# Kernel optimization log

Hardware: AMD Instinct MI355X
Metric: run time of the kernel (lower is better)

Reference implementation:

```python
import jax, jax.numpy as jnp
import numpy as np

NUM_LOCAL = 4      # num_local_experts
E_TOTAL = 8        # local + unpopular experts
HIDDEN = 1024
FFN = 4 * HIDDEN
CAP = 2048         # tokens (capacity) per expert
D0 = 1             # leading dim of inputs / output_tensor


def setup_inputs() -> dict:
    key = jax.random.key(0)
    k_in, k_w0, k_w3 = jax.random.split(key, 3)
    inputs = jax.random.normal(k_in, (D0, E_TOTAL, CAP, HIDDEN), dtype=jnp.float32)
    # gating-activity indicator per expert; all-ones -> all unpopular experts active
    output_tensor = jnp.ones((D0, E_TOTAL), dtype=jnp.float32)
    # stacked per-expert MLP weights (torch Linear convention: [out, in])
    w0 = jax.random.normal(k_w0, (E_TOTAL, FFN, HIDDEN), dtype=jnp.float32) * 0.02
    w3 = jax.random.normal(k_w3, (E_TOTAL, HIDDEN, FFN), dtype=jnp.float32) * 0.02
    return {"output_tensor": output_tensor, "inputs": inputs, "w0": w0, "w3": w3}


def reference(output_tensor, inputs, w0, w3):
    # Grouped 2-layer MLP per expert: x @ w0^T -> GELU -> @ w3^T
    # b: D0, e: expert, c: capacity, d: hidden, f: ffn
    h = jnp.einsum('becd,efd->becf', inputs, w0)
    h = jax.nn.gelu(h, approximate=False)  # torch nn.GELU default = exact erf
    out = jnp.einsum('becf,edf->becd', h, w3)
    # unpopular experts with zero activity produce zeros (scatter-into-zeros combine)
    unpop_mask = jnp.sum(output_tensor[:, NUM_LOCAL:], axis=0) != 0  # [E_unpop]
    full_mask = jnp.concatenate(
        [jnp.ones((NUM_LOCAL,), dtype=bool), unpop_mask])  # locals always computed
    out = out * full_mask[None, :, None, None].astype(out.dtype)
    return out
```

## Files before the change

### kernel.cpp

```cpp
#include <hip/hip_runtime.h>
#include <math.h>

#define E_TOTAL 8
#define NUM_LOCAL 4
#define HIDDEN 1024
#define FFN 4096
#define CAP 2048

typedef unsigned short ushort_t;
typedef __attribute__((ext_vector_type(8))) short short8;
typedef __attribute__((ext_vector_type(8))) unsigned short u16x8;
typedef __attribute__((ext_vector_type(4))) float f32x4;

__device__ __forceinline__ unsigned short f2bf(float f) {
  unsigned int u = __float_as_uint(f);
  u += 0x7FFFu + ((u >> 16) & 1u);
  return (unsigned short)(u >> 16);
}

__device__ __forceinline__ void gload_lds16(const void* g, void* l) {
  __builtin_amdgcn_global_load_lds(
      (const __attribute__((address_space(1))) void*)g,
      (__attribute__((address_space(3))) void*)l,
      16, 0, 0);
}

__global__ __launch_bounds__(256) void cvt_kernel(const float4* __restrict__ s,
                                                  u16x8* __restrict__ d) {
  const size_t i = (size_t)blockIdx.x * 256 + threadIdx.x;
  float4 a = s[2 * i], b = s[2 * i + 1];
  u16x8 o;
  o[0] = f2bf(a.x); o[1] = f2bf(a.y); o[2] = f2bf(a.z); o[3] = f2bf(a.w);
  o[4] = f2bf(b.x); o[5] = f2bf(b.y); o[6] = f2bf(b.z); o[7] = f2bf(b.w);
  d[i] = o;
}

template <int M, int N, int K, bool GELU_OUT>
__global__ __launch_bounds__(256, 2) void gemm_nt(
    const ushort_t* __restrict__ A, const ushort_t* __restrict__ B,
    void* __restrict__ Cout, const float* __restrict__ ot, int d0) {
  __shared__ ushort_t lds_a[128 * 64];
  __shared__ ushort_t lds_b[128 * 64];

  const int e = blockIdx.z;
  const int bm = blockIdx.x * 128;
  const int bn = blockIdx.y * 128;
  const int t = threadIdx.x;
  const int wave = t >> 6, lane = t & 63;
  const int wr = wave >> 1, wc = wave & 1;
  const int quad = lane >> 4, l16 = lane & 15;
  const int r8 = lane >> 3;
  const int s8 = lane & 7;
  const int g8 = (s8 + r8) & 7;

  const ushort_t* Ag = A + (size_t)e * M * K + (size_t)(bm + r8) * K + g8 * 8;
  const ushort_t* Bg = B + (size_t)e * N * K + (size_t)(bn + r8) * K + g8 * 8;

  f32x4 acc[4][4];
#pragma unroll
  for (int i = 0; i < 4; ++i)
#pragma unroll
    for (int j = 0; j < 4; ++j) {
      f32x4 z = {0.f, 0.f, 0.f, 0.f};
      acc[i][j] = z;
    }

  for (int kb = 0; kb < K / 64; ++kb) {
    const size_t ko = (size_t)kb * 64;
#pragma unroll
    for (int j = 0; j < 4; ++j) {
      const int R = (j * 4 + wave) * 8;
      gload_lds16(Ag + ko + (size_t)R * K, &lds_a[R * 64]);
      gload_lds16(Bg + ko + (size_t)R * K, &lds_b[R * 64]);
    }
    __syncthreads();

#pragma unroll
    for (int ks = 0; ks < 2; ++ks) {
      short8 af[4], bfr[4];
      const int c = ks * 4 + quad;
#pragma unroll
      for (int i = 0; i < 4; ++i) {
        const int ra = wr * 64 + i * 16 + l16;
        const int rb = wc * 64 + i * 16 + l16;
        af[i]  = *(const short8*)&lds_a[ra * 64 + ((c - ra) & 7) * 8];
        bfr[i] = *(const short8*)&lds_b[rb * 64 + ((c - rb) & 7) * 8];
      }
#pragma unroll
      for (int mi = 0; mi < 4; ++mi)
#pragma unroll
        for (int ni = 0; ni < 4; ++ni)
          acc[mi][ni] = __builtin_amdgcn_mfma_f32_16x16x32_bf16(
              af[mi], bfr[ni], acc[mi][ni], 0, 0, 0);
    }
    __syncthreads();
  }

  if (GELU_OUT) {
    ushort_t* C = (ushort_t*)Cout + (size_t)e * M * N +
                  (size_t)(bm + wr * 64) * N + (bn + wc * 64);
#pragma unroll
    for (int mi = 0; mi < 4; ++mi)
#pragma unroll
      for (int r = 0; r < 4; ++r) {
        const int row = mi * 16 + quad * 4 + r;
#pragma unroll
        for (int ni = 0; ni < 4; ++ni) {
          float v = acc[mi][ni][r];
          v = 0.5f * v * (1.f + erff(v * 0.70710678118654752f));
          C[(size_t)row * N + ni * 16 + l16] = f2bf(v);
        }
      }
  } else {
    float mask = 1.f;
    if (e >= NUM_LOCAL) {
      float s = 0.f;
      for (int b = 0; b < d0; ++b) s += ot[b * E_TOTAL + e];
      mask = (s != 0.f) ? 1.f : 0.f;
    }
    float* C = (float*)Cout + (size_t)e * M * N +
               (size_t)(bm + wr * 64) * N + (bn + wc * 64);
#pragma unroll
    for (int mi = 0; mi < 4; ++mi)
#pragma unroll
      for (int r = 0; r < 4; ++r) {
        const int row = mi * 16 + quad * 4 + r;
#pragma unroll
        for (int ni = 0; ni < 4; ++ni)
          C[(size_t)row * N + ni * 16 + l16] = acc[mi][ni][r] * mask;
      }
  }
}

extern "C" void kernel_launch(void* const* d_in, const int* in_sizes, int n_in,
                              void* d_out, int out_size, void* d_ws,
                              size_t ws_size, hipStream_t stream) {
  const float* ot = (const float*)d_in[0];
  const float* x  = (const float*)d_in[1];
  const float* w0 = (const float*)d_in[2];
  const float* w3 = (const float*)d_in[3];
  const int d0 = in_sizes[0] / E_TOTAL;

  char* ws = (char*)d_ws;
  ushort_t* xb  = (ushort_t*)ws;
  ushort_t* w0b = (ushort_t*)(ws + (size_t)32 * 1024 * 1024);
  ushort_t* w3b = (ushort_t*)ws;
  ushort_t* h   = (ushort_t*)(ws + (size_t)96 * 1024 * 1024);

  const int nx = E_TOTAL * CAP * HIDDEN;
  const int nw = E_TOTAL * FFN * HIDDEN;

  cvt_kernel<<<nx / (256 * 8), 256, 0, stream>>>((const float4*)x, (u16x8*)xb);
  cvt_kernel<<<nw / (256 * 8), 256, 0, stream>>>((const float4*)w0, (u16x8*)w0b);

  gemm_nt<CAP, FFN, HIDDEN, true>
      <<<dim3(CAP / 128, FFN / 128, E_TOTAL), 256, 0, stream>>>(
          xb, w0b, h, nullptr, d0);

  cvt_kernel<<<nw / (256 * 8), 256, 0, stream>>>((const float4*)w3, (u16x8*)w3b);

  gemm_nt<CAP, HIDDEN, FFN, false>
      <<<dim3(CAP / 128, HIDDEN / 128, E_TOTAL), 256, 0, stream>>>(
          h, w3b, d_out, ot, d0);
}
```

Measured before the change: 677.0 us.

## Switch GEMMs to 32x32x16 MFMA and merge bf16 conversions into one kernel

The GEMM inner loop now issues 32x32x16 bf16 MFMA instructions on 2x2 accumulator tiles instead of 16x16x32 on 4x4 tiles. That halves the LDS fragment loads per MFMA and uses the larger matrix-core op, with the epilogue index mapping rewritten to match. When the workspace is large enough, the three fp32-to-bf16 conversions run as one kernel with separate buffers, which removes two launches. The 32-wide output stores have a different coalescing pattern, and the larger workspace path depends on ws_size.

```diff
diff --git a/kernel.cpp b/kernel.cpp
--- a/kernel.cpp
+++ b/kernel.cpp
@@ -10,7 +10,7 @@
 typedef unsigned short ushort_t;
 typedef __attribute__((ext_vector_type(8))) short short8;
 typedef __attribute__((ext_vector_type(8))) unsigned short u16x8;
-typedef __attribute__((ext_vector_type(4))) float f32x4;
+typedef __attribute__((ext_vector_type(16))) float f32x16;
 
 __device__ __forceinline__ unsigned short f2bf(float f) {
   unsigned int u = __float_as_uint(f);
@@ -23,6 +23,26 @@
       (const __attribute__((address_space(1))) void*)g,
       (__attribute__((address_space(3))) void*)l,
       16, 0, 0);
+}
+
+__global__ __launch_bounds__(256) void cvt3_kernel(
+    const float4* __restrict__ x, const float4* __restrict__ w0,
+    const float4* __restrict__ w3, u16x8* __restrict__ xb,
+    u16x8* __restrict__ w0b, u16x8* __restrict__ w3b) {
+  const int NX8 = E_TOTAL * CAP * HIDDEN / 8;
+  const int NW8 = E_TOTAL * FFN * HIDDEN / 8;
+  const int i = blockIdx.x * 256 + threadIdx.x;
+  const float4* s;
+  u16x8* d;
+  int j;
+  if (i < NX8) { s = x; d = xb; j = i; }
+  else if (i < NX8 + NW8) { s = w0; d = w0b; j = i - NX8; }
+  else { s = w3; d = w3b; j = i - NX8 - NW8; }
+  float4 a = s[2 * (size_t)j], b = s[2 * (size_t)j + 1];
+  u16x8 o;
+  o[0] = f2bf(a.x); o[1] = f2bf(a.y); o[2] = f2bf(a.z); o[3] = f2bf(a.w);
+  o[4] = f2bf(b.x); o[5] = f2bf(b.y); o[6] = f2bf(b.z); o[7] = f2bf(b.w);
+  d[j] = o;
 }
 
 __global__ __launch_bounds__(256) void cvt_kernel(const float4* __restrict__ s,
@@ -48,7 +68,7 @@
   const int t = threadIdx.x;
   const int wave = t >> 6, lane = t & 63;
   const int wr = wave >> 1, wc = wave & 1;
-  const int quad = lane >> 4, l16 = lane & 15;
+  const int l32 = lane & 31, h5 = lane >> 5;
   const int r8 = lane >> 3;
   const int s8 = lane & 7;
   const int g8 = (s8 + r8) & 7;
@@ -56,14 +76,13 @@
   const ushort_t* Ag = A + (size_t)e * M * K + (size_t)(bm + r8) * K + g8 * 8;
   const ushort_t* Bg = B + (size_t)e * N * K + (size_t)(bn + r8) * K + g8 * 8;
 
-  f32x4 acc[4][4];
-#pragma unroll
-  for (int i = 0; i < 4; ++i)
-#pragma unroll
-    for (int j = 0; j < 4; ++j) {
-      f32x4 z = {0.f, 0.f, 0.f, 0.f};
-      acc[i][j] = z;
-    }
+  f32x16 acc[2][2];
+#pragma unroll
+  for (int i = 0; i < 2; ++i)
+#pragma unroll
+    for (int j = 0; j < 2; ++j)
+#pragma unroll
+      for (int r = 0; r < 16; ++r) acc[i][j][r] = 0.f;
 
   for (int kb = 0; kb < K / 64; ++kb) {
     const size_t ko = (size_t)kb * 64;
@@ -76,39 +95,40 @@
     __syncthreads();
 
 #pragma unroll
-    for (int ks = 0; ks < 2; ++ks) {
-      short8 af[4], bfr[4];
-      const int c = ks * 4 + quad;
-#pragma unroll
-      for (int i = 0; i < 4; ++i) {
-        const int ra = wr * 64 + i * 16 + l16;
-        const int rb = wc * 64 + i * 16 + l16;
-        af[i]  = *(const short8*)&lds_a[ra * 64 + ((c - ra) & 7) * 8];
-        bfr[i] = *(const short8*)&lds_b[rb * 64 + ((c - rb) & 7) * 8];
+    for (int ks = 0; ks < 4; ++ks) {
+      const int c = ks * 2 + h5;
+      short8 af[2], bfr[2];
+#pragma unroll
+      for (int mi = 0; mi < 2; ++mi) {
+        const int ra = wr * 64 + mi * 32 + l32;
+        const int rb = wc * 64 + mi * 32 + l32;
+        af[mi]  = *(const short8*)&lds_a[ra * 64 + ((c - ra) & 7) * 8];
+        bfr[mi] = *(const short8*)&lds_b[rb * 64 + ((c - rb) & 7) * 8];
       }
 #pragma unroll
-      for (int mi = 0; mi < 4; ++mi)
-#pragma unroll
-        for (int ni = 0; ni < 4; ++ni)
-          acc[mi][ni] = __builtin_amdgcn_mfma_f32_16x16x32_bf16(
+      for (int mi = 0; mi < 2; ++mi)
+#pragma unroll
+        for (int ni = 0; ni < 2; ++ni)
+          acc[mi][ni] = __builtin_amdgcn_mfma_f32_32x32x16_bf16(
               af[mi], bfr[ni], acc[mi][ni], 0, 0, 0);
     }
     __syncthreads();
   }
 
   if (GELU_OUT) {
-    ushort_t* C = (ushort_t*)Cout + (size_t)e * M * N +
-                  (size_t)(bm + wr * 64) * N + (bn + wc * 64);
-#pragma unroll
-    for (int mi = 0; mi < 4; ++mi)
-#pragma unroll
-      for (int r = 0; r < 4; ++r) {
-        const int row = mi * 16 + quad * 4 + r;
-#pragma unroll
-        for (int ni = 0; ni < 4; ++ni) {
+    ushort_t* C = (ushort_t*)Cout + (size_t)e * M * N;
+#pragma unroll
+    for (int mi = 0; mi < 2; ++mi)
+#pragma unroll
+      for (int ni = 0; ni < 2; ++ni) {
+        const int rbase = bm + wr * 64 + mi * 32;
+        const int cbase = bn + wc * 64 + ni * 32;
+#pragma unroll
+        for (int r = 0; r < 16; ++r) {
+          const int row = rbase + (r & 3) + 8 * (r >> 2) + 4 * h5;
           float v = acc[mi][ni][r];
           v = 0.5f * v * (1.f + erff(v * 0.70710678118654752f));
-          C[(size_t)row * N + ni * 16 + l16] = f2bf(v);
+          C[(size_t)row * N + cbase + l32] = f2bf(v);
         }
       }
   } else {
@@ -118,16 +138,18 @@
       for (int b = 0; b < d0; ++b) s += ot[b * E_TOTAL + e];
       mask = (s != 0.f) ? 1.f : 0.f;
     }
-    float* C = (float*)Cout + (size_t)e * M * N +
-               (size_t)(bm + wr * 64) * N + (bn + wc * 64);
-#pragma unroll
-    for (int mi = 0; mi < 4; ++mi)
-#pragma unroll
-      for (int r = 0; r < 4; ++r) {
-        const int row = mi * 16 + quad * 4 + r;
-#pragma unroll
-        for (int ni = 0; ni < 4; ++ni)
-          C[(size_t)row * N + ni * 16 + l16] = acc[mi][ni][r] * mask;
+    float* C = (float*)Cout + (size_t)e * M * N;
+#pragma unroll
+    for (int mi = 0; mi < 2; ++mi)
+#pragma unroll
+      for (int ni = 0; ni < 2; ++ni) {
+        const int rbase = bm + wr * 64 + mi * 32;
+        const int cbase = bn + wc * 64 + ni * 32;
+#pragma unroll
+        for (int r = 0; r < 16; ++r) {
+          const int row = rbase + (r & 3) + 8 * (r >> 2) + 4 * h5;
+          C[(size_t)row * N + cbase + l32] = acc[mi][ni][r] * mask;
+        }
       }
   }
 }
@@ -142,24 +164,43 @@
   const int d0 = in_sizes[0] / E_TOTAL;
 
   char* ws = (char*)d_ws;
-  ushort_t* xb  = (ushort_t*)ws;
-  ushort_t* w0b = (ushort_t*)(ws + (size_t)32 * 1024 * 1024);
-  ushort_t* w3b = (ushort_t*)ws;
-  ushort_t* h   = (ushort_t*)(ws + (size_t)96 * 1024 * 1024);
-
+  const size_t MB = 1024 * 1024;
   const int nx = E_TOTAL * CAP * HIDDEN;
   const int nw = E_TOTAL * FFN * HIDDEN;
 
-  cvt_kernel<<<nx / (256 * 8), 256, 0, stream>>>((const float4*)x, (u16x8*)xb);
-  cvt_kernel<<<nw / (256 * 8), 256, 0, stream>>>((const float4*)w0, (u16x8*)w0b);
-
-  gemm_nt<CAP, FFN, HIDDEN, true>
-      <<<dim3(CAP / 128, FFN / 128, E_TOTAL), 256, 0, stream>>>(
-          xb, w0b, h, nullptr, d0);
-
-  cvt_kernel<<<nw / (256 * 8), 256, 0, stream>>>((const float4*)w3, (u16x8*)w3b);
-
-  gemm_nt<CAP, HIDDEN, FFN, false>
-      <<<dim3(CAP / 128, HIDDEN / 128, E_TOTAL), 256, 0, stream>>>(
-          h, w3b, d_out, ot, d0);
-}
+  if (ws_size >= 288 * MB) {
+    ushort_t* xb  = (ushort_t*)ws;
+    ushort_t* w0b = (ushort_t*)(ws + 32 * MB);
+    ushort_t* w3b = (ushort_t*)(ws + 96 * MB);
+    ushort_t* h   = (ushort_t*)(ws + 160 * MB);
+
+    cvt3_kernel<<<(nx + 2 * nw) / (256 * 8), 256, 0, stream>>>(
+        (const float4*)x, (const float4*)w0, (const float4*)w3,
+        (u16x8*)xb, (u16x8*)w0b, (u16x8*)w3b);
+
+    gemm_nt<CAP, FFN, HIDDEN, true>
+        <<<dim3(CAP / 128, FFN / 128, E_TOTAL), 256, 0, stream>>>(
+            xb, w0b, h, nullptr, d0);
+    gemm_nt<CAP, HIDDEN, FFN, false>
+        <<<dim3(CAP / 128, HIDDEN / 128, E_TOTAL), 256, 0, stream>>>(
+            h, w3b, d_out, ot, d0);
+  } else {
+    ushort_t* xb  = (ushort_t*)ws;
+    ushort_t* w0b = (ushort_t*)(ws + 32 * MB);
+    ushort_t* w3b = (ushort_t*)ws;
+    ushort_t* h   = (ushort_t*)(ws + 96 * MB);
+
+    cvt_kernel<<<nx / (256 * 8), 256, 0, stream>>>((const float4*)x,
+                                                   (u16x8*)xb);
+    cvt_kernel<<<nw / (256 * 8), 256, 0, stream>>>((const float4*)w0,
+                                                   (u16x8*)w0b);
+    gemm_nt<CAP, FFN, HIDDEN, true>
+        <<<dim3(CAP / 128, FFN / 128, E_TOTAL), 256, 0, stream>>>(
+            xb, w0b, h, nullptr, d0);
+    cvt_kernel<<<nw / (256 * 8), 256, 0, stream>>>((const float4*)w3,
+                                                   (u16x8*)w3b);
+    gemm_nt<CAP, HIDDEN, FFN, false>
+        <<<dim3(CAP / 128, HIDDEN / 128, E_TOTAL), 256, 0, stream>>>(
+            h, w3b, d_out, ot, d0);
+  }
+}
```

Result: slower. 693.0 us (+2.4%).
